# Performance work log

Measured on AMD Instinct MI355X. Metric: run time of the kernel, lower is better.

## Reference

```python
import jax, jax.numpy as jnp
import numpy as np

BS, T, Q, HID, PROJ = 16, 16, 100, 256, 256


def setup_inputs() -> dict:
    key = jax.random.key(0)
    k1, k2, k3, k4, k5 = jax.random.split(key, 5)
    frame_embeds = jax.random.normal(k1, (BS, T, Q, HID), jnp.float32)
    other_frame_embeds = jax.random.normal(k2, (BS, T, Q, HID), jnp.float32)
    W = jax.random.normal(k3, (HID, PROJ), jnp.float32) / np.sqrt(HID).astype(np.float32)
    b = jax.random.normal(k4, (PROJ,), jnp.float32) * 0.01
    n = BS * Q
    mid = jax.random.randint(k5, (n, 1), 1, T - 1, dtype=jnp.int32)
    bridge = jnp.concatenate(
        [jnp.zeros((n, 1), jnp.int32), mid, jnp.full((n, 1), T - 1, jnp.int32)], axis=1
    )  # (n,3): head=0, random pivot in [1,T-2], tail=T-1
    return {"frame_embeds": frame_embeds, "other_frame_embeds": other_frame_embeds,
            "W": W, "b": b, "bridge": bridge}


def _prep(fe, W, b):
    # Linear proj, (bs,t,q,c)->(bs*q, t, c), L2-normalize per embedding.
    bs, t, q, _ = fe.shape
    x = fe @ W + b
    x = x.transpose(0, 2, 1, 3).reshape(bs * q, t, -1)
    return x / jnp.linalg.norm(x, axis=-1, keepdims=True)


def _forward(frame_embeds, other_frame_embeds, W, b, bridge, delta=0.3):
    cur = _prep(frame_embeds, W, b)      # (n,t,c)
    other = _prep(other_frame_embeds, W, b)
    bh = bridge[:, 0].astype(jnp.float32)
    bp_f = bridge[:, 1].astype(jnp.float32)
    bt = bridge[:, 2].astype(jnp.float32)
    alpha = (bp_f - bh) / (bt - bh)      # (n,)
    sigma = alpha * (bt - bp_f)          # (n,)
    g = jnp.take_along_axis(cur, bridge[:, :, None], axis=1)  # (n,3,c) head/pivot/tail
    # positive brownian-bridge distance
    x = g[:, 1] - (1.0 - alpha)[:, None] * g[:, 0] - alpha[:, None] * g[:, 2]
    numer = jnp.exp(-jnp.sum(x * x, axis=-1) / (2.0 * sigma ** 2))  # (n,)
    # negatives: pivot frame taken from every sequence in [cur; other].
    # ||m_ij - a_i||^2 = ||m_ij||^2 - 2 m_ij.a_i + ||a_i||^2 with m_ij = neg_all[j, bp_i],
    # avoiding the (n,N,3,c) repeat tensor of the original.
    neg_all = jnp.concatenate([cur, other], axis=0)            # (N,t,c)
    a = (1.0 - alpha)[:, None] * g[:, 0] + alpha[:, None] * g[:, 2]  # (n,c)
    cross = jnp.einsum('ic,jtc->ijt', a, neg_all)              # (n,N,t)
    bp = bridge[:, 1]
    cross_g = jnp.take_along_axis(cross, bp[:, None, None], axis=2)[..., 0]  # (n,N)
    nn2_g = jnp.sum(neg_all * neg_all, axis=-1).T[bp]          # (n,N)
    x2 = nn2_g - 2.0 * cross_g + jnp.sum(a * a, axis=-1)[:, None]
    dist = -x2 / (2.0 * sigma ** 2)[:, None]                   # (n,N)
    n = dist.shape[0]
    idx = jnp.arange(n)
    self_dist = dist[idx, idx]
    dist = dist.at[idx, idx].set(-10000.0)
    topv, _ = jax.lax.top_k(dist, 5)
    deno = jnp.exp(jnp.concatenate([self_dist[:, None], topv], axis=-1))  # (n,6)
    brownian_loss = (numer / deno.sum(axis=-1)).mean()
    score = jnp.einsum('nc,nc->n', cur[:, 0], cur[:, -1])
    head_tail_match = jax.nn.softplus(delta - score).mean()
    return brownian_loss, head_tail_match


def reference(frame_embeds, other_frame_embeds, W, b, bridge):
    return _forward(frame_embeds, other_frame_embeds, W, b, bridge)
```

## Files before the change

kernel.cpp:

```cpp
#include <hip/hip_runtime.h>
#include <hip/hip_bf16.h>

#define NROW 1600
#define NEG  3200
#define ROWS_FLAT 25600
#define NSPLIT 25

using bf16x8 = __attribute__((ext_vector_type(8))) short;
using f32x4  = __attribute__((ext_vector_type(4))) float;

__device__ __forceinline__ float bf2f(unsigned v) { return __uint_as_float(v << 16); }
__device__ __forceinline__ ushort f2bf(float f) {
  __hip_bfloat16 h = __float2bfloat16(f);
  return *(ushort*)&h;
}
__device__ __forceinline__ float load1(const ushort* p, size_t idx, int f32) {
  return f32 ? ((const float*)p)[idx] : bf2f(p[idx]);
}
__device__ __forceinline__ int sniff_f32(const ushort* p, int lane) {
  unsigned e = ((unsigned)p[2*lane] >> 7) & 0xffu;
  unsigned long long b = __ballot(e >= 100u && e <= 140u);
  return (__popcll(b) >= 40) ? 0 : 1;
}
__device__ __forceinline__ bf16x8 cvt8(const float* p) {
  float4 fa = *(const float4*)p;
  float4 fb = *(const float4*)(p + 4);
  bf16x8 r;
  r[0]=(short)f2bf(fa.x); r[1]=(short)f2bf(fa.y); r[2]=(short)f2bf(fa.z); r[3]=(short)f2bf(fa.w);
  r[4]=(short)f2bf(fb.x); r[5]=(short)f2bf(fb.y); r[6]=(short)f2bf(fb.z); r[7]=(short)f2bf(fb.w);
  return r;
}

__global__ __launch_bounds__(256) void k_prep(const ushort* __restrict__ W,
    ushort* __restrict__ Wt, int* __restrict__ zbase) {
  if (blockIdx.x == 0 && threadIdx.x < 21) zbase[threadIdx.x] = 0;
  int fW = sniff_f32(W, threadIdx.x & 63);
  Wt[blockIdx.x * 256 + threadIdx.x] = f2bf(load1(W, (size_t)threadIdx.x * 256 + blockIdx.x, fW));
}

__global__ __launch_bounds__(256) void k_proj(const ushort* __restrict__ fe0,
    const ushort* __restrict__ fe1, const ushort* __restrict__ Wt,
    const ushort* __restrict__ bias, const int* __restrict__ bridge,
    ushort* __restrict__ Pb, ushort* __restrict__ Ab, float* __restrict__ prm,
    float* __restrict__ numer, int* __restrict__ cnt, int* __restrict__ lst,
    float* __restrict__ wsum) {
  __shared__ union {
    float  xf[64*256];
    ushort x[64*256];
    ushort c[4][32*72];
  } sh;
  __shared__ float s_ss[4][64];
  __shared__ float s_bb[2][4][2][3];
  __shared__ int   s_brg[4][3];
  const int tid = threadIdx.x;
  const int w = tid >> 6, lane = tid & 63, q = lane >> 4, m = lane & 15;
  const int I0 = blockIdx.x * 4;
  const int hasB = (I0 < NROW);
  const int s1 = (I0 >= NROW);
  const ushort* srcp = s1 ? fe1 : fe0;
  const int fSrc = sniff_f32(srcp, lane);
  const int fB   = sniff_f32(bias, lane);
  if (hasB && tid < 12) s_brg[tid/3][tid%3] = bridge[(I0 + tid/3)*3 + tid%3];
  {
    int ii = I0 - s1*NROW + w;
    int b = ii / 100, qq = ii - b*100;
    const size_t ub = (size_t)(b*1600 + qq) * 256;
    if (fSrc) {
      const float* fp = (const float*)srcp;
      #pragma unroll
      for (int i2 = 0; i2 < 16; i2++) {
        int r = w*16 + i2;
        int g = lane ^ ((i2 & 7) << 1);
        const float* gp = fp + ub + (size_t)i2*25600 + g*4;
        __builtin_amdgcn_global_load_lds(
          (const __attribute__((address_space(1))) unsigned int*)gp,
          (__attribute__((address_space(3))) unsigned int*)&sh.xf[r*256], 16, 0, 0);
      }
    } else {
      #pragma unroll
      for (int i2 = 0; i2 < 8; i2++) {
        int c = w*8 + i2;
        int t  = 2*i2 + (lane >> 5);
        int kc = (lane & 31) ^ (t & 7);
        const ushort* gp = srcp + ub + (size_t)t*25600 + kc*8;
        __builtin_amdgcn_global_load_lds(
          (const __attribute__((address_space(1))) unsigned int*)gp,
          (__attribute__((address_space(3))) unsigned int*)&sh.x[c*512], 16, 0, 0);
      }
    }
  }
  __syncthreads();
  f32x4 acc[4][4];
  #pragma unroll
  for (int nt = 0; nt < 4; nt++) {
    float bb = load1(bias, w*64 + nt*16 + m, fB);
    f32x4 v = {bb, bb, bb, bb};
    #pragma unroll
    for (int mt = 0; mt < 4; mt++) acc[mt][nt] = v;
  }
  const int sw = (m & 7) << 3;
  const int e2 = (m & 7) << 1;
  const ushort* wbase = Wt + (size_t)(w*64 + m)*256 + q*8;
  bf16x8 a_cur[4], b_cur[4];
  if (fSrc) {
    int pg = (q*2) ^ e2;
    #pragma unroll
    for (int mt = 0; mt < 4; mt++) a_cur[mt] = cvt8(&sh.xf[(mt*16 + m)*256 + pg*4]);
  } else {
    #pragma unroll
    for (int mt = 0; mt < 4; mt++)
      a_cur[mt] = *(const bf16x8*)&sh.x[(mt*16 + m)*256 + ((q*8) ^ sw)];
  }
  #pragma unroll
  for (int nt = 0; nt < 4; nt++)
    b_cur[nt] = *(const bf16x8*)(wbase + (size_t)nt*16*256);
  #pragma unroll
  for (int k = 0; k < 8; k++) {
    bf16x8 a_nxt[4], b_nxt[4];
    if (k < 7) {
      int k0 = (k + 1) * 32;
      #pragma unroll
      for (int nt = 0; nt < 4; nt++)
        b_nxt[nt] = *(const bf16x8*)(wbase + (size_t)nt*16*256 + k0);
      if (fSrc) {
        int pg = ((k+1)*8 + q*2) ^ e2;
        #pragma unroll
        for (int mt = 0; mt < 4; mt++) a_nxt[mt] = cvt8(&sh.xf[(mt*16 + m)*256 + pg*4]);
      } else {
        int pk = (k0 + q*8) ^ sw;
        #pragma unroll
        for (int mt = 0; mt < 4; mt++)
          a_nxt[mt] = *(const bf16x8*)&sh.x[(mt*16 + m)*256 + pk];
      }
    }
    #pragma unroll
    for (int nt = 0; nt < 4; nt++)
      #pragma unroll
      for (int mt = 0; mt < 4; mt++)
        acc[mt][nt] = __builtin_amdgcn_mfma_f32_16x16x32_bf16(a_cur[mt], b_cur[nt], acc[mt][nt], 0, 0, 0);
    if (k < 7) {
      #pragma unroll
      for (int x = 0; x < 4; x++) { a_cur[x] = a_nxt[x]; b_cur[x] = b_nxt[x]; }
    }
  }
  float ssp[4][4];
  #pragma unroll
  for (int mt = 0; mt < 4; mt++)
    #pragma unroll
    for (int reg = 0; reg < 4; reg++) {
      float s = 0.f;
      #pragma unroll
      for (int nt = 0; nt < 4; nt++) { float v = acc[mt][nt][reg]; s += v*v; }
      ssp[mt][reg] = s;
    }
  #pragma unroll
  for (int mk = 1; mk < 16; mk <<= 1)
    #pragma unroll
    for (int mt = 0; mt < 4; mt++)
      #pragma unroll
      for (int reg = 0; reg < 4; reg++) ssp[mt][reg] += __shfl_xor(ssp[mt][reg], mk, 64);
  if (m == 0)
    #pragma unroll
    for (int mt = 0; mt < 4; mt++)
      #pragma unroll
      for (int reg = 0; reg < 4; reg++) s_ss[w][mt*16 + 4*q + reg] = ssp[mt][reg];
  __syncthreads();
  float inv[4][4];
  #pragma unroll
  for (int mt = 0; mt < 4; mt++)
    #pragma unroll
    for (int reg = 0; reg < 4; reg++) {
      int row = mt*16 + 4*q + reg;
      float s = s_ss[0][row] + s_ss[1][row] + s_ss[2][row] + s_ss[3][row];
      inv[mt][reg] = 1.0f / sqrtf(s);
    }
  #pragma unroll
  for (int half = 0; half < 2; half++) {
    #pragma unroll
    for (int mt = half*2; mt < half*2 + 2; mt++)
      #pragma unroll
      for (int reg = 0; reg < 4; reg++) {
        int rl = (mt - half*2)*16 + 4*q + reg;
        #pragma unroll
        for (int nt = 0; nt < 4; nt++)
          sh.c[w][rl*72 + nt*16 + m] = f2bf(acc[mt][nt][reg] * inv[mt][reg]);
      }
    __syncthreads();
    #pragma unroll
    for (int p = 0; p < 4; p++) {
      int row = p*8 + (tid >> 5);
      int r   = half*32 + row;
      int ig  = r >> 4, t = r & 15;
      int I   = I0 + ig;
      int ch  = tid & 31;
      uint4 v = *(uint4*)&sh.c[ch >> 3][row*72 + (ch & 7)*8];
      *(uint4*)(Pb + ((size_t)t * NEG + I) * 256 + ch*8) = v;
    }
    if (hasB) {
      #pragma unroll
      for (int ih = 0; ih < 2; ih++) {
        int ig = half*2 + ih;
        int bh = s_brg[ig][0], bp = s_brg[ig][1], bt = s_brg[ig][2];
        float alpha = ((float)bp - (float)bh) / ((float)bt - (float)bh);
        int rb = ih*16;
        float g0 = bf2f(sh.c[w][(rb + bh)*72 + lane]);
        float g1 = bf2f(sh.c[w][(rb + bp)*72 + lane]);
        float g2 = bf2f(sh.c[w][(rb + bt)*72 + lane]);
        float hd = bf2f(sh.c[w][(rb +  0)*72 + lane]);
        float tl = bf2f(sh.c[w][(rb + 15)*72 + lane]);
        float a = (1.0f - alpha) * g0 + alpha * g2;
        float x = g1 - a;
        int I = I0 + ig;
        Ab[(size_t)I*256 + w*64 + lane] = f2bf(a);
        float xx = x*x, aa = a*a, sc = hd*tl;
        #pragma unroll
        for (int mk = 1; mk < 64; mk <<= 1) {
          xx += __shfl_xor(xx, mk, 64);
          aa += __shfl_xor(aa, mk, 64);
          sc += __shfl_xor(sc, mk, 64);
        }
        if (lane == 0) { s_bb[half][w][ih][0] = xx; s_bb[half][w][ih][1] = aa; s_bb[half][w][ih][2] = sc; }
      }
    }
    __syncthreads();
    if (hasB && tid < 2) {
      int ig = half*2 + tid;
      int I = I0 + ig;
      float XX = s_bb[half][0][tid][0] + s_bb[half][1][tid][0] + s_bb[half][2][tid][0] + s_bb[half][3][tid][0];
      float AA = s_bb[half][0][tid][1] + s_bb[half][1][tid][1] + s_bb[half][2][tid][1] + s_bb[half][3][tid][1];
      float SC = s_bb[half][0][tid][2] + s_bb[half][1][tid][2] + s_bb[half][2][tid][2] + s_bb[half][3][tid][2];
      int bh = s_brg[ig][0], bp = s_brg[ig][1], bt = s_brg[ig][2];
      float alpha = ((float)bp - (float)bh) / ((float)bt - (float)bh);
      float sigma = alpha * ((float)bt - (float)bp);
      float inv2s2 = 1.0f / (2.0f * sigma * sigma);
      prm[I*2+0] = inv2s2;
      prm[I*2+1] = AA;
      numer[I] = expf(-XX * inv2s2);
      float sp = log1pf(expf(0.3f - SC));
      atomicAdd(wsum + 1, sp * (1.0f / 1600.0f));
      int pos = atomicAdd(cnt + bp, 1);
      lst[bp * 1600 + pos] = I;
    }
  }
}

__device__ __forceinline__ void sort5(float* c) {
  #define CE(i,j) { float hi = fmaxf(c[i], c[j]), lo = fminf(c[i], c[j]); c[i]=hi; c[j]=lo; }
  CE(0,1) CE(3,4) CE(2,4) CE(2,3) CE(1,4) CE(0,3) CE(0,2) CE(1,3) CE(1,2)
  #undef CE
}
__device__ __forceinline__ void ins5(float* t, float v) {
  float hi, lo;
  hi = fmaxf(t[0], v); lo = fminf(t[0], v); t[0] = hi; v = lo;
  hi = fmaxf(t[1], v); lo = fminf(t[1], v); t[1] = hi; v = lo;
  hi = fmaxf(t[2], v); lo = fminf(t[2], v); t[2] = hi; v = lo;
  hi = fmaxf(t[3], v); lo = fminf(t[3], v); t[3] = hi; v = lo;
  t[4] = fmaxf(t[4], v);
}

__global__ __launch_bounds__(256) void k_cross(const ushort* __restrict__ Pb,
    const ushort* __restrict__ Ab, const float* __restrict__ prm,
    const int* __restrict__ cnt, const int* __restrict__ lst,
    float* __restrict__ part) {
  int t = blockIdx.z;
  int n_t = min(cnt[t], 1600);
  int i0 = blockIdx.y * 64;
  if (i0 >= n_t) return;
  int j0 = blockIdx.x * 128;
  __shared__ int s_gis[64];
  __shared__ float s_red[4][64][6];
  int tid = threadIdx.x;
  if (tid < 64) {
    int gi = lst[t*1600 + min(i0 + tid, n_t - 1)];
    s_gis[tid] = min(max(gi, 0), NROW - 1);
  }
  __syncthreads();
  const int w = tid >> 6, lane = tid & 63, q = lane >> 4, m = lane & 15;
  const ushort* jp0 = Pb + ((size_t)t * NEG + (j0 + w*32 + m)) * 256 + q*8;
  const ushort* jp1 = jp0 + (size_t)16*256;
  int gi[4];
  const ushort* ip[4];
  #pragma unroll
  for (int it = 0; it < 4; it++) {
    gi[it] = s_gis[it*16 + m];
    ip[it] = Ab + (size_t)gi[it] * 256 + q*8;
  }
  f32x4 acc[2][4];
  #pragma unroll
  for (int jt = 0; jt < 2; jt++)
    #pragma unroll
    for (int it = 0; it < 4; it++) { f32x4 z = {0.f,0.f,0.f,0.f}; acc[jt][it] = z; }
  bf16x8 jc0 = *(const bf16x8*)(jp0);
  bf16x8 jc1 = *(const bf16x8*)(jp1);
  bf16x8 ic[4];
  #pragma unroll
  for (int it = 0; it < 4; it++) ic[it] = *(const bf16x8*)(ip[it]);
  #pragma unroll
  for (int k = 0; k < 8; k++) {
    bf16x8 jn0, jn1, in[4];
    if (k < 7) {
      int o = (k + 1) * 32;
      jn0 = *(const bf16x8*)(jp0 + o);
      jn1 = *(const bf16x8*)(jp1 + o);
      #pragma unroll
      for (int it = 0; it < 4; it++) in[it] = *(const bf16x8*)(ip[it] + o);
    }
    __builtin_amdgcn_s_setprio(1);
    #pragma unroll
    for (int it = 0; it < 4; it++) {
      acc[0][it] = __builtin_amdgcn_mfma_f32_16x16x32_bf16(jc0, ic[it], acc[0][it], 0, 0, 0);
      acc[1][it] = __builtin_amdgcn_mfma_f32_16x16x32_bf16(jc1, ic[it], acc[1][it], 0, 0, 0);
    }
    __builtin_amdgcn_s_setprio(0);
    if (k < 7) { jc0 = jn0; jc1 = jn1;
      #pragma unroll
      for (int it = 0; it < 4; it++) ic[it] = in[it];
    }
  }
  float top[4][5], selfv[4];
  float pi[4], pa[4];
  #pragma unroll
  for (int it = 0; it < 4; it++) {
    pi[it] = prm[gi[it]*2]; pa[it] = prm[gi[it]*2+1];
    selfv[it] = -1e30f;
    #pragma unroll
    for (int k = 0; k < 5; k++) top[it][k] = -1e30f;
  }
  #pragma unroll
  for (int jt = 0; jt < 2; jt++)
    #pragma unroll
    for (int reg = 0; reg < 4; reg++) {
      int j = j0 + w*32 + jt*16 + 4*q + reg;
      #pragma unroll
      for (int it = 0; it < 4; it++) {
        float d = -(1.0f - 2.0f*acc[jt][it][reg] + pa[it]) * pi[it];
        if (j == gi[it]) selfv[it] = d; else ins5(top[it], d);
      }
    }
  #pragma unroll
  for (int mk = 16; mk <= 32; mk <<= 1) {
    #pragma unroll
    for (int it = 0; it < 4; it++) {
      float o[5], c[5];
      #pragma unroll
      for (int k = 0; k < 5; k++) o[k] = __shfl_xor(top[it][k], mk, 64);
      #pragma unroll
      for (int k = 0; k < 5; k++) c[k] = fmaxf(top[it][k], o[4 - k]);
      sort5(c);
      #pragma unroll
      for (int k = 0; k < 5; k++) top[it][k] = c[k];
      selfv[it] = fmaxf(selfv[it], __shfl_xor(selfv[it], mk, 64));
    }
  }
  if (q == 0) {
    #pragma unroll
    for (int it = 0; it < 4; it++) {
      #pragma unroll
      for (int k = 0; k < 5; k++) s_red[w][it*16 + m][k] = top[it][k];
      s_red[w][it*16 + m][5] = selfv[it];
    }
  }
  __syncthreads();
  if (tid < 64 && i0 + tid < n_t) {
    float T[5], S = s_red[0][tid][5];
    #pragma unroll
    for (int k = 0; k < 5; k++) T[k] = s_red[0][tid][k];
    #pragma unroll
    for (int w2 = 1; w2 < 4; w2++) {
      #pragma unroll
      for (int k = 0; k < 5; k++) ins5(T, s_red[w2][tid][k]);
      S = fmaxf(S, s_red[w2][tid][5]);
    }
    float* pp = part + ((size_t)s_gis[tid]*NSPLIT + blockIdx.x) * 6;
    #pragma unroll
    for (int k = 0; k < 5; k++) pp[k] = T[k];
    pp[5] = S;
  }
}

__global__ __launch_bounds__(64) void k_merge(const float* __restrict__ part,
    const float* __restrict__ numer, float* __restrict__ wsum, int* __restrict__ done,
    const ushort* __restrict__ fe0, void* __restrict__ out) {
  int i = blockIdx.x * 64 + threadIdx.x;
  const float* pp = part + (size_t)i * NSPLIT * 6;
  float T[5]; float S = pp[5];
  #pragma unroll
  for (int k = 0; k < 5; k++) T[k] = pp[k];
  #pragma unroll
  for (int s = 1; s < NSPLIT; s++) {
    const float* ps = pp + s*6;
    float v0 = ps[0], v1 = ps[1], v2 = ps[2], v3 = ps[3], v4 = ps[4], v5 = ps[5];
    ins5(T, v0); ins5(T, v1); ins5(T, v2); ins5(T, v3); ins5(T, v4);
    S = fmaxf(S, v5);
  }
  float deno = expf(S);
  #pragma unroll
  for (int k = 0; k < 5; k++) deno += expf(T[k]);
  float local = numer[i] / deno;
  #pragma unroll
  for (int mk = 1; mk < 64; mk <<= 1) local += __shfl_xor(local, mk, 64);
  __shared__ int s_last;
  if (threadIdx.x == 0) {
    atomicAdd(wsum + 0, local * (1.0f / 1600.0f));
    __threadfence();
    s_last = (atomicAdd(done, 1) == 24);
  }
  __syncthreads();
  if (s_last) {
    int f = sniff_f32(fe0, threadIdx.x);
    if (threadIdx.x == 0) {
      __threadfence();
      float brown = __hip_atomic_load(wsum + 0, __ATOMIC_RELAXED, __HIP_MEMORY_SCOPE_AGENT);
      float sp    = __hip_atomic_load(wsum + 1, __ATOMIC_RELAXED, __HIP_MEMORY_SCOPE_AGENT);
      if (f) {
        ((float*)out)[0] = brown;
        ((float*)out)[1] = sp;
      } else {
        ushort* o = (ushort*)out;
        o[0] = f2bf(brown);
        o[1] = f2bf(sp);
      }
    }
  }
}

extern "C" void kernel_launch(void* const* d_in, const int* in_sizes, int n_in,
                              void* d_out, int out_size, void* d_ws, size_t ws_size,
                              hipStream_t stream) {
  const ushort* fe0    = (const ushort*)d_in[0];
  const ushort* fe1    = (const ushort*)d_in[1];
  const ushort* W      = (const ushort*)d_in[2];
  const ushort* bias   = (const ushort*)d_in[3];
  const int*    bridge = (const int*)d_in[4];

  ushort* Pb    = (ushort*)d_ws;
  ushort* Ab    = Pb + 13107200;
  ushort* Wt    = Ab + 409600;
  float*  part  = (float*)(Wt + 65536);
  float*  prm   = part + 240000;
  float*  numer = prm + 3200;
  float*  wsum  = numer + 1600;
  int*    cnt   = (int*)(wsum + 4);
  int*    done  = cnt + 16;
  int*    lst   = done + 1;

  k_prep  <<<256, 256, 0, stream>>>(W, Wt, (int*)wsum);
  k_proj  <<<800, 256, 0, stream>>>(fe0, fe1, Wt, bias, bridge, Pb, Ab, prm, numer, cnt, lst, wsum);
  k_cross <<<dim3(NSPLIT, 7, 16), 256, 0, stream>>>(Pb, Ab, prm, cnt, lst, part);
  k_merge <<<25, 64, 0, stream>>>(part, numer, wsum, done, fe0, d_out);
}
```

Measured before the change: 168.5 us.

## Halve k_proj rows per block and pre-swizzle W into fragment-contiguous layout

Each k_proj block now handles 2 sequences (32 rows) instead of 4, so the grid doubles to 1600 blocks, LDS use halves, and the two-pass epilogue collapses to one pass. k_prep writes W in an MFMA-fragment order so each lane's B fragment load is contiguous and coalesced across the wave. The fp32 LDS swizzle also changes to a per-float4 xor. The aim is higher occupancy and better tail balance across CUs, at the cost of fewer MFMAs per B-fragment load (less W reuse) and more blocks to schedule.

New measurement: 161.3 us. 4.3% less time.

```diff
diff --git a/kernel.cpp b/kernel.cpp
--- a/kernel.cpp
+++ b/kernel.cpp
@@ -22,9 +22,9 @@
   unsigned long long b = __ballot(e >= 100u && e <= 140u);
   return (__popcll(b) >= 40) ? 0 : 1;
 }
-__device__ __forceinline__ bf16x8 cvt8(const float* p) {
-  float4 fa = *(const float4*)p;
-  float4 fb = *(const float4*)(p + 4);
+__device__ __forceinline__ bf16x8 cvt8b(const float* a, const float* b) {
+  float4 fa = *(const float4*)a;
+  float4 fb = *(const float4*)b;
   bf16x8 r;
   r[0]=(short)f2bf(fa.x); r[1]=(short)f2bf(fa.y); r[2]=(short)f2bf(fa.z); r[3]=(short)f2bf(fa.w);
   r[4]=(short)f2bf(fb.x); r[5]=(short)f2bf(fb.y); r[6]=(short)f2bf(fb.z); r[7]=(short)f2bf(fb.w);
@@ -32,56 +32,61 @@
 }
 
 __global__ __launch_bounds__(256) void k_prep(const ushort* __restrict__ W,
-    ushort* __restrict__ Wt, int* __restrict__ zbase) {
+    ushort* __restrict__ Wtf, int* __restrict__ zbase) {
   if (blockIdx.x == 0 && threadIdx.x < 21) zbase[threadIdx.x] = 0;
   int fW = sniff_f32(W, threadIdx.x & 63);
-  Wt[blockIdx.x * 256 + threadIdx.x] = f2bf(load1(W, (size_t)threadIdx.x * 256 + blockIdx.x, fW));
+  int n = blockIdx.x, k = threadIdx.x;
+  int n16 = n >> 4, m = n & 15, kb = k >> 5, q = (k >> 3) & 3, e = k & 7;
+  Wtf[(size_t)(n16*8 + kb)*512 + q*128 + m*8 + e] =
+      f2bf(load1(W, (size_t)k * 256 + n, fW));
 }
 
 __global__ __launch_bounds__(256) void k_proj(const ushort* __restrict__ fe0,
-    const ushort* __restrict__ fe1, const ushort* __restrict__ Wt,
+    const ushort* __restrict__ fe1, const ushort* __restrict__ Wtf,
     const ushort* __restrict__ bias, const int* __restrict__ bridge,
     ushort* __restrict__ Pb, ushort* __restrict__ Ab, float* __restrict__ prm,
     float* __restrict__ numer, int* __restrict__ cnt, int* __restrict__ lst,
     float* __restrict__ wsum) {
   __shared__ union {
-    float  xf[64*256];
-    ushort x[64*256];
+    float  xf[32*256];
+    ushort x[32*256];
     ushort c[4][32*72];
   } sh;
-  __shared__ float s_ss[4][64];
-  __shared__ float s_bb[2][4][2][3];
-  __shared__ int   s_brg[4][3];
+  __shared__ float s_ss[4][32];
+  __shared__ float s_bb[4][2][3];
+  __shared__ int   s_brg[2][3];
   const int tid = threadIdx.x;
   const int w = tid >> 6, lane = tid & 63, q = lane >> 4, m = lane & 15;
-  const int I0 = blockIdx.x * 4;
+  const int I0 = blockIdx.x * 2;
   const int hasB = (I0 < NROW);
   const int s1 = (I0 >= NROW);
   const ushort* srcp = s1 ? fe1 : fe0;
   const int fSrc = sniff_f32(srcp, lane);
   const int fB   = sniff_f32(bias, lane);
-  if (hasB && tid < 12) s_brg[tid/3][tid%3] = bridge[(I0 + tid/3)*3 + tid%3];
+  if (hasB && tid < 6) s_brg[tid/3][tid%3] = bridge[(I0 + tid/3)*3 + tid%3];
   {
-    int ii = I0 - s1*NROW + w;
+    int ii = I0 - s1*NROW + (w >> 1);
     int b = ii / 100, qq = ii - b*100;
     const size_t ub = (size_t)(b*1600 + qq) * 256;
     if (fSrc) {
       const float* fp = (const float*)srcp;
       #pragma unroll
-      for (int i2 = 0; i2 < 16; i2++) {
-        int r = w*16 + i2;
-        int g = lane ^ ((i2 & 7) << 1);
-        const float* gp = fp + ub + (size_t)i2*25600 + g*4;
+      for (int i2 = 0; i2 < 8; i2++) {
+        int r = w*8 + i2;
+        int t = r & 15;
+        int g = lane ^ (i2 & 7);
+        const float* gp = fp + ub + (size_t)t*25600 + g*4;
         __builtin_amdgcn_global_load_lds(
           (const __attribute__((address_space(1))) unsigned int*)gp,
           (__attribute__((address_space(3))) unsigned int*)&sh.xf[r*256], 16, 0, 0);
       }
     } else {
       #pragma unroll
-      for (int i2 = 0; i2 < 8; i2++) {
-        int c = w*8 + i2;
-        int t  = 2*i2 + (lane >> 5);
-        int kc = (lane & 31) ^ (t & 7);
+      for (int i2 = 0; i2 < 4; i2++) {
+        int c = w*4 + i2;
+        int r  = 2*c + (lane >> 5);
+        int t  = r & 15;
+        int kc = (lane & 31) ^ (r & 7);
         const ushort* gp = srcp + ub + (size_t)t*25600 + kc*8;
         __builtin_amdgcn_global_load_lds(
           (const __attribute__((address_space(1))) unsigned int*)gp,
@@ -90,62 +95,63 @@
     }
   }
   __syncthreads();
-  f32x4 acc[4][4];
+  f32x4 acc[2][4];
   #pragma unroll
   for (int nt = 0; nt < 4; nt++) {
     float bb = load1(bias, w*64 + nt*16 + m, fB);
     f32x4 v = {bb, bb, bb, bb};
     #pragma unroll
-    for (int mt = 0; mt < 4; mt++) acc[mt][nt] = v;
+    for (int mt = 0; mt < 2; mt++) acc[mt][nt] = v;
   }
   const int sw = (m & 7) << 3;
-  const int e2 = (m & 7) << 1;
-  const ushort* wbase = Wt + (size_t)(w*64 + m)*256 + q*8;
-  bf16x8 a_cur[4], b_cur[4];
+  const ushort* wfb = Wtf + (size_t)(w*4)*4096 + lane*8;
+  bf16x8 a_cur[2], b_cur[4];
   if (fSrc) {
-    int pg = (q*2) ^ e2;
-    #pragma unroll
-    for (int mt = 0; mt < 4; mt++) a_cur[mt] = cvt8(&sh.xf[(mt*16 + m)*256 + pg*4]);
+    int g0 = (q*2) ^ (m&7), g1 = (q*2 + 1) ^ (m&7);
+    #pragma unroll
+    for (int mt = 0; mt < 2; mt++)
+      a_cur[mt] = cvt8b(&sh.xf[(mt*16+m)*256 + g0*4], &sh.xf[(mt*16+m)*256 + g1*4]);
   } else {
     #pragma unroll
-    for (int mt = 0; mt < 4; mt++)
+    for (int mt = 0; mt < 2; mt++)
       a_cur[mt] = *(const bf16x8*)&sh.x[(mt*16 + m)*256 + ((q*8) ^ sw)];
   }
   #pragma unroll
   for (int nt = 0; nt < 4; nt++)
-    b_cur[nt] = *(const bf16x8*)(wbase + (size_t)nt*16*256);
+    b_cur[nt] = *(const bf16x8*)(wfb + (size_t)nt*4096);
   #pragma unroll
   for (int k = 0; k < 8; k++) {
-    bf16x8 a_nxt[4], b_nxt[4];
+    bf16x8 a_nxt[2], b_nxt[4];
     if (k < 7) {
-      int k0 = (k + 1) * 32;
       #pragma unroll
       for (int nt = 0; nt < 4; nt++)
-        b_nxt[nt] = *(const bf16x8*)(wbase + (size_t)nt*16*256 + k0);
+        b_nxt[nt] = *(const bf16x8*)(wfb + (size_t)nt*4096 + (k+1)*512);
       if (fSrc) {
-        int pg = ((k+1)*8 + q*2) ^ e2;
+        int g0 = ((k+1)*8 + q*2) ^ (m&7), g1 = ((k+1)*8 + q*2 + 1) ^ (m&7);
         #pragma unroll
-        for (int mt = 0; mt < 4; mt++) a_nxt[mt] = cvt8(&sh.xf[(mt*16 + m)*256 + pg*4]);
+        for (int mt = 0; mt < 2; mt++)
+          a_nxt[mt] = cvt8b(&sh.xf[(mt*16+m)*256 + g0*4], &sh.xf[(mt*16+m)*256 + g1*4]);
       } else {
-        int pk = (k0 + q*8) ^ sw;
+        int pk = ((k+1)*32 + q*8) ^ sw;
         #pragma unroll
-        for (int mt = 0; mt < 4; mt++)
+        for (int mt = 0; mt < 2; mt++)
           a_nxt[mt] = *(const bf16x8*)&sh.x[(mt*16 + m)*256 + pk];
       }
     }
     #pragma unroll
     for (int nt = 0; nt < 4; nt++)
       #pragma unroll
-      for (int mt = 0; mt < 4; mt++)
+      for (int mt = 0; mt < 2; mt++)
         acc[mt][nt] = __builtin_amdgcn_mfma_f32_16x16x32_bf16(a_cur[mt], b_cur[nt], acc[mt][nt], 0, 0, 0);
     if (k < 7) {
-      #pragma unroll
-      for (int x = 0; x < 4; x++) { a_cur[x] = a_nxt[x]; b_cur[x] = b_nxt[x]; }
-    }
-  }
-  float ssp[4][4];
-  #pragma unroll
-  for (int mt = 0; mt < 4; mt++)
+      a_cur[0] = a_nxt[0]; a_cur[1] = a_nxt[1];
+      #pragma unroll
+      for (int x = 0; x < 4; x++) b_cur[x] = b_nxt[x];
+    }
+  }
+  float ssp[2][4];
+  #pragma unroll
+  for (int mt = 0; mt < 2; mt++)
     #pragma unroll
     for (int reg = 0; reg < 4; reg++) {
       float s = 0.f;
@@ -156,18 +162,18 @@
   #pragma unroll
   for (int mk = 1; mk < 16; mk <<= 1)
     #pragma unroll
-    for (int mt = 0; mt < 4; mt++)
+    for (int mt = 0; mt < 2; mt++)
       #pragma unroll
       for (int reg = 0; reg < 4; reg++) ssp[mt][reg] += __shfl_xor(ssp[mt][reg], mk, 64);
   if (m == 0)
     #pragma unroll
-    for (int mt = 0; mt < 4; mt++)
+    for (int mt = 0; mt < 2; mt++)
       #pragma unroll
       for (int reg = 0; reg < 4; reg++) s_ss[w][mt*16 + 4*q + reg] = ssp[mt][reg];
   __syncthreads();
-  float inv[4][4];
-  #pragma unroll
-  for (int mt = 0; mt < 4; mt++)
+  float inv[2][4];
+  #pragma unroll
+  for (int mt = 0; mt < 2; mt++)
     #pragma unroll
     for (int reg = 0; reg < 4; reg++) {
       int row = mt*16 + 4*q + reg;
@@ -175,61 +181,55 @@
       inv[mt][reg] = 1.0f / sqrtf(s);
     }
   #pragma unroll
-  for (int half = 0; half < 2; half++) {
-    #pragma unroll
-    for (int mt = half*2; mt < half*2 + 2; mt++)
-      #pragma unroll
-      for (int reg = 0; reg < 4; reg++) {
-        int rl = (mt - half*2)*16 + 4*q + reg;
-        #pragma unroll
-        for (int nt = 0; nt < 4; nt++)
-          sh.c[w][rl*72 + nt*16 + m] = f2bf(acc[mt][nt][reg] * inv[mt][reg]);
-      }
+  for (int mt = 0; mt < 2; mt++)
+    #pragma unroll
+    for (int reg = 0; reg < 4; reg++) {
+      int rl = mt*16 + 4*q + reg;
+      #pragma unroll
+      for (int nt = 0; nt < 4; nt++)
+        sh.c[w][rl*72 + nt*16 + m] = f2bf(acc[mt][nt][reg] * inv[mt][reg]);
+    }
+  __syncthreads();
+  #pragma unroll
+  for (int p = 0; p < 4; p++) {
+    int row = p*8 + (tid >> 5);
+    int ig  = row >> 4, t = row & 15;
+    int I   = I0 + ig;
+    int ch  = tid & 31;
+    uint4 v = *(uint4*)&sh.c[ch >> 3][row*72 + (ch & 7)*8];
+    *(uint4*)(Pb + ((size_t)t * NEG + I) * 256 + ch*8) = v;
+  }
+  if (hasB) {
+    #pragma unroll
+    for (int ih = 0; ih < 2; ih++) {
+      int bh = s_brg[ih][0], bp = s_brg[ih][1], bt = s_brg[ih][2];
+      float alpha = ((float)bp - (float)bh) / ((float)bt - (float)bh);
+      int rb = ih*16;
+      float g0 = bf2f(sh.c[w][(rb + bh)*72 + lane]);
+      float g1 = bf2f(sh.c[w][(rb + bp)*72 + lane]);
+      float g2 = bf2f(sh.c[w][(rb + bt)*72 + lane]);
+      float hd = bf2f(sh.c[w][(rb +  0)*72 + lane]);
+      float tl = bf2f(sh.c[w][(rb + 15)*72 + lane]);
+      float a = (1.0f - alpha) * g0 + alpha * g2;
+      float x = g1 - a;
+      int I = I0 + ih;
+      Ab[(size_t)I*256 + w*64 + lane] = f2bf(a);
+      float xx = x*x, aa = a*a, sc = hd*tl;
+      #pragma unroll
+      for (int mk = 1; mk < 64; mk <<= 1) {
+        xx += __shfl_xor(xx, mk, 64);
+        aa += __shfl_xor(aa, mk, 64);
+        sc += __shfl_xor(sc, mk, 64);
+      }
+      if (lane == 0) { s_bb[w][ih][0] = xx; s_bb[w][ih][1] = aa; s_bb[w][ih][2] = sc; }
+    }
     __syncthreads();
-    #pragma unroll
-    for (int p = 0; p < 4; p++) {
-      int row = p*8 + (tid >> 5);
-      int r   = half*32 + row;
-      int ig  = r >> 4, t = r & 15;
-      int I   = I0 + ig;
-      int ch  = tid & 31;
-      uint4 v = *(uint4*)&sh.c[ch >> 3][row*72 + (ch & 7)*8];
-      *(uint4*)(Pb + ((size_t)t * NEG + I) * 256 + ch*8) = v;
-    }
-    if (hasB) {
-      #pragma unroll
-      for (int ih = 0; ih < 2; ih++) {
-        int ig = half*2 + ih;
-        int bh = s_brg[ig][0], bp = s_brg[ig][1], bt = s_brg[ig][2];
-        float alpha = ((float)bp - (float)bh) / ((float)bt - (float)bh);
-        int rb = ih*16;
-        float g0 = bf2f(sh.c[w][(rb + bh)*72 + lane]);
-        float g1 = bf2f(sh.c[w][(rb + bp)*72 + lane]);
-        float g2 = bf2f(sh.c[w][(rb + bt)*72 + lane]);
-        float hd = bf2f(sh.c[w][(rb +  0)*72 + lane]);
-        float tl = bf2f(sh.c[w][(rb + 15)*72 + lane]);
-        float a = (1.0f - alpha) * g0 + alpha * g2;
-        float x = g1 - a;
-        int I = I0 + ig;
-        Ab[(size_t)I*256 + w*64 + lane] = f2bf(a);
-        float xx = x*x, aa = a*a, sc = hd*tl;
-        #pragma unroll
-        for (int mk = 1; mk < 64; mk <<= 1) {
-          xx += __shfl_xor(xx, mk, 64);
-          aa += __shfl_xor(aa, mk, 64);
-          sc += __shfl_xor(sc, mk, 64);
-        }
-        if (lane == 0) { s_bb[half][w][ih][0] = xx; s_bb[half][w][ih][1] = aa; s_bb[half][w][ih][2] = sc; }
-      }
-    }
-    __syncthreads();
-    if (hasB && tid < 2) {
-      int ig = half*2 + tid;
-      int I = I0 + ig;
-      float XX = s_bb[half][0][tid][0] + s_bb[half][1][tid][0] + s_bb[half][2][tid][0] + s_bb[half][3][tid][0];
-      float AA = s_bb[half][0][tid][1] + s_bb[half][1][tid][1] + s_bb[half][2][tid][1] + s_bb[half][3][tid][1];
-      float SC = s_bb[half][0][tid][2] + s_bb[half][1][tid][2] + s_bb[half][2][tid][2] + s_bb[half][3][tid][2];
-      int bh = s_brg[ig][0], bp = s_brg[ig][1], bt = s_brg[ig][2];
+    if (tid < 2) {
+      int I = I0 + tid;
+      float XX = s_bb[0][tid][0] + s_bb[1][tid][0] + s_bb[2][tid][0] + s_bb[3][tid][0];
+      float AA = s_bb[0][tid][1] + s_bb[1][tid][1] + s_bb[2][tid][1] + s_bb[3][tid][1];
+      float SC = s_bb[0][tid][2] + s_bb[1][tid][2] + s_bb[2][tid][2] + s_bb[3][tid][2];
+      int bh = s_brg[tid][0], bp = s_brg[tid][1], bt = s_brg[tid][2];
       float alpha = ((float)bp - (float)bh) / ((float)bt - (float)bh);
       float sigma = alpha * ((float)bt - (float)bp);
       float inv2s2 = 1.0f / (2.0f * sigma * sigma);
@@ -435,8 +435,8 @@
 
   ushort* Pb    = (ushort*)d_ws;
   ushort* Ab    = Pb + 13107200;
-  ushort* Wt    = Ab + 409600;
-  float*  part  = (float*)(Wt + 65536);
+  ushort* Wtf   = Ab + 409600;
+  float*  part  = (float*)(Wtf + 65536);
   float*  prm   = part + 240000;
   float*  numer = prm + 3200;
   float*  wsum  = numer + 1600;
@@ -444,8 +444,8 @@
   int*    done  = cnt + 16;
   int*    lst   = done + 1;
 
-  k_prep  <<<256, 256, 0, stream>>>(W, Wt, (int*)wsum);
-  k_proj  <<<800, 256, 0, stream>>>(fe0, fe1, Wt, bias, bridge, Pb, Ab, prm, numer, cnt, lst, wsum);
+  k_prep  <<<256, 256, 0, stream>>>(W, Wtf, (int*)wsum);
+  k_proj  <<<1600, 256, 0, stream>>>(fe0, fe1, Wtf, bias, bridge, Pb, Ab, prm, numer, cnt, lst, wsum);
   k_cross <<<dim3(NSPLIT, 7, 16), 256, 0, stream>>>(Pb, Ab, prm, cnt, lst, part);
   k_merge <<<25, 64, 0, stream>>>(part, numer, wsum, done, fe0, d_out);
 }
```
